# Optimization experiments

Hardware: AMD Instinct MI355X
Metric: run time of the kernel (lower is better)

## Reference

```python
import jax, jax.numpy as jnp
import numpy as np

C, H, W, N = 256, 256, 256, 512
ROI_SIZE = 7


def setup_inputs() -> dict:
    key = jax.random.key(0)
    k1, k2, k3 = jax.random.split(key, 3)
    feature = jax.random.normal(k1, (C, H, W), dtype=jnp.float32)
    # rois layout: (y1, x1, y2, x2), valid boxes inside the map
    start = jax.random.uniform(k2, (N, 2), jnp.float32, 0.0, H / 2)
    size = jax.random.uniform(k3, (N, 2), jnp.float32, 8.0, H / 2)
    rois = jnp.concatenate([start, start + size], axis=-1)
    return {"feature": feature, "rois": rois}


def _bilinear(feature, x, y):
    # feature: [C, H, W]; x, y: [...] float sample coords.
    # Faithful to the torch code: corners are clamped BEFORE computing the
    # interpolation weights (y - y1, y2 - y, etc.).
    h, w = feature.shape[-2:]
    y1 = jnp.floor(y).astype(jnp.int32)
    y2 = y1 + 1
    x1 = jnp.floor(x).astype(jnp.int32)
    x2 = x1 + 1
    y1 = jnp.clip(y1, 0, h - 1)
    y2 = jnp.clip(y2, 0, h - 1)
    x1 = jnp.clip(x1, 0, w - 1)
    x2 = jnp.clip(x2, 0, w - 1)
    wy1 = y - y1  # dist to top (clamped) corner
    wy2 = y2 - y
    wx1 = x - x1
    wx2 = x2 - x
    f11 = feature[:, y1, x1]  # [C, ...]
    f12 = feature[:, y1, x2]
    f21 = feature[:, y2, x1]
    f22 = feature[:, y2, x2]
    p = f11 * wx2 + f12 * wx1
    q = f21 * wx2 + f22 * wx1
    return p * wy2 + q * wy1


def reference(feature, rois):
    # feature: [C, H, W]; rois: [N, 4] = (y1, x1, y2, x2)
    R = ROI_SIZE
    n_roi = rois.shape[0]
    c = feature.shape[0]
    stride_h = (rois[:, 2] - rois[:, 0]) / R  # [N]
    stride_w = (rois[:, 3] - rois[:, 1]) / R  # [N]
    bins = jnp.arange(R, dtype=feature.dtype)
    y_base = rois[:, 0, None] + stride_h[:, None] * bins  # [N, 7]
    x_base = rois[:, 1, None] + stride_w[:, None] * bins  # [N, 7]
    # two sample points per bin, at 1/3 and 2/3 of the bin stride
    ys = jnp.stack([y_base + stride_h[:, None] / 3,
                    y_base + 2 * stride_h[:, None] / 3], axis=-1)  # [N, 7, 2]
    xs = jnp.stack([x_base + stride_w[:, None] / 3,
                    x_base + 2 * stride_w[:, None] / 3], axis=-1)  # [N, 7, 2]
    # all (y_sample, x_sample) combos per (roi, bin_m, bin_n): [N, 7, 7, 2, 2]
    Y = ys[:, :, None, :, None]
    X = xs[:, None, :, None, :]
    Yb, Xb = jnp.broadcast_arrays(Y, X)
    vals = _bilinear(feature, Xb, Yb)  # [C, N, 7, 7, 2, 2]
    # Faithful to torch.max(cat(...)) on a [C, 4] tensor: a GLOBAL max over
    # both channels and the 4 sample points, broadcast back to all channels.
    pooled = vals.max(axis=(0, -2, -1))  # [N, 7, 7]
    return jnp.broadcast_to(pooled[:, None, :, :], (n_roi, c, R, R))
```

## Files before the change

kernel.cpp:

```cpp
#include <hip/hip_runtime.h>

#define CCH 256
#define HH  256
#define WW  256
#define HWSZ (HH * WW)
#define NROI 512
#define RBIN 7
#define NBIN (RBIN * RBIN)
#define NTASK (2 * NBIN)
#define TFEAT_BYTES ((size_t)HWSZ * CCH * 2)

typedef float vfloat4 __attribute__((ext_vector_type(4)));

__device__ __forceinline__ unsigned short f2bf_rne(float f) {
    unsigned u = __float_as_uint(f);
    u = (u + 0x7fffu + ((u >> 16) & 1u)) >> 16;
    return (unsigned short)u;
}

__global__ __launch_bounds__(256)
void transpose_chw_to_hwc_bf16(const float* __restrict__ feat,
                               unsigned short* __restrict__ tfeat)
{
    __shared__ __align__(16) float tile[64 * 64];
    const int t   = threadIdx.x;
    const int hw0 = blockIdx.x * 64;
    const int c0  = blockIdx.y * 64;

    const int cl_r = t >> 4;
    const int fc   = t & 15;

    vfloat4 v[4];
    #pragma unroll
    for (int j = 0; j < 4; ++j) {
        v[j] = __builtin_nontemporal_load(
            (const vfloat4*)(feat + (size_t)(c0 + cl_r + j * 16) * HWSZ + hw0 + 4 * fc));
    }
    #pragma unroll
    for (int j = 0; j < 4; ++j) {
        const int cl = cl_r + j * 16;
        const int p  = (4 * fc) ^ (4 * ((cl >> 2) & 7));
        *(vfloat4*)&tile[cl * 64 + p] = v[j];
    }
    __syncthreads();

    const int cl_w = (t & 15) * 4;
    const int swz  = 4 * ((t & 15) & 7);
    #pragma unroll
    for (int j = 0; j < 4; ++j) {
        const int hl = (t >> 4) + j * 16;
        const int pc = hl ^ swz;
        ushort4 w;
        w.x = f2bf_rne(tile[(cl_w + 0) * 64 + pc]);
        w.y = f2bf_rne(tile[(cl_w + 1) * 64 + pc]);
        w.z = f2bf_rne(tile[(cl_w + 2) * 64 + pc]);
        w.w = f2bf_rne(tile[(cl_w + 3) * 64 + pc]);
        *(ushort4*)(tfeat + (size_t)(hw0 + hl) * CCH + c0 + cl_w) = w;
    }
}

__global__ __launch_bounds__(1024, 8)
void roialign_fused(const unsigned short* __restrict__ tfeat,
                    const float* __restrict__ rois,
                    float* __restrict__ out)
{
    const int n    = blockIdx.x;
    const int t    = threadIdx.x;
    const int wave = t >> 6;
    const int lane = t & 63;
    const int half = lane >> 5;
    const int cOff = (lane & 31) * 8;

    __shared__ __align__(16) float tmax[NTASK * 64];
    __shared__ float pooled[NBIN];

    const float y0 = rois[n * 4 + 0];
    const float x0 = rois[n * 4 + 1];
    const float sh = (rois[n * 4 + 2] - y0) * (1.0f / (float)RBIN);
    const float sw = (rois[n * 4 + 3] - x0) * (1.0f / (float)RBIN);

    #pragma unroll 2
    for (int task = wave; task < NTASK; task += 16) {
        const int bin = task >> 1;
        const int i   = task & 1;
        const int by  = bin / RBIN;
        const int bx  = bin - by * RBIN;

        const int point = i * 2 + half;
        const int sy = point >> 1;
        const int sx = point & 1;

        const float y = y0 + sh * (float)by +
                        ((sy == 0) ? (sh * (1.0f / 3.0f)) : (sh * (2.0f / 3.0f)));
        const float x = x0 + sw * (float)bx +
                        ((sx == 0) ? (sw * (1.0f / 3.0f)) : (sw * (2.0f / 3.0f)));

        int iy1 = (int)floorf(y);
        int iy2 = iy1 + 1;
        int ix1 = (int)floorf(x);
        int ix2 = ix1 + 1;
        iy1 = min(max(iy1, 0), HH - 1);
        iy2 = min(max(iy2, 0), HH - 1);
        ix1 = min(max(ix1, 0), WW - 1);
        ix2 = min(max(ix2, 0), WW - 1);

        const float wy1 = y - (float)iy1;
        const float wy2 = (float)iy2 - y;
        const float wx1 = x - (float)ix1;
        const float wx2 = (float)ix2 - x;

        const uint4 A = *(const uint4*)(tfeat + (size_t)(iy1 * WW + ix1) * CCH + cOff);
        const uint4 B = *(const uint4*)(tfeat + (size_t)(iy1 * WW + ix2) * CCH + cOff);
        const uint4 C = *(const uint4*)(tfeat + (size_t)(iy2 * WW + ix1) * CCH + cOff);
        const uint4 D = *(const uint4*)(tfeat + (size_t)(iy2 * WW + ix2) * CCH + cOff);
        const unsigned* ap = (const unsigned*)&A;
        const unsigned* bp = (const unsigned*)&B;
        const unsigned* cp = (const unsigned*)&C;
        const unsigned* dp = (const unsigned*)&D;

        float m = -INFINITY;
        #pragma unroll
        for (int k = 0; k < 4; ++k) {
            const unsigned ua = ap[k], ub = bp[k], uc = cp[k], ud = dp[k];
            {
                const float f11 = __uint_as_float(ua << 16);
                const float f12 = __uint_as_float(ub << 16);
                const float f21 = __uint_as_float(uc << 16);
                const float f22 = __uint_as_float(ud << 16);
                const float p = f11 * wx2 + f12 * wx1;
                const float q = f21 * wx2 + f22 * wx1;
                m = fmaxf(m, p * wy2 + q * wy1);
            }
            {
                const float f11 = __uint_as_float(ua & 0xffff0000u);
                const float f12 = __uint_as_float(ub & 0xffff0000u);
                const float f21 = __uint_as_float(uc & 0xffff0000u);
                const float f22 = __uint_as_float(ud & 0xffff0000u);
                const float p = f11 * wx2 + f12 * wx1;
                const float q = f21 * wx2 + f22 * wx1;
                m = fmaxf(m, p * wy2 + q * wy1);
            }
        }

        tmax[task * 64 + lane] = m;
    }
    __syncthreads();

    if (t < NBIN * 16) {
        const int b = t >> 4;
        const int j = t & 15;
        const float* src = &tmax[b * 128 + j * 8];
        const vfloat4 a = *(const vfloat4*)(src);
        const vfloat4 c = *(const vfloat4*)(src + 4);
        float m = fmaxf(fmaxf(fmaxf(a.x, a.y), fmaxf(a.z, a.w)),
                        fmaxf(fmaxf(c.x, c.y), fmaxf(c.z, c.w)));
        #pragma unroll
        for (int off = 8; off > 0; off >>= 1)
            m = fmaxf(m, __shfl_xor(m, off, 16));
        if (j == 0) pooled[b] = m;
    }
    __syncthreads();

    float* o = out + (size_t)n * (CCH * NBIN);
    #pragma unroll
    for (int k = 0; k < 4; ++k) {
        const int idx4 = t + k * 1024;
        if (idx4 < (CCH * NBIN) / 4) {
            int r = (idx4 * 4) % NBIN;
            vfloat4 v;
            v.x = pooled[r]; r = (r == NBIN - 1) ? 0 : r + 1;
            v.y = pooled[r]; r = (r == NBIN - 1) ? 0 : r + 1;
            v.z = pooled[r]; r = (r == NBIN - 1) ? 0 : r + 1;
            v.w = pooled[r];
            __builtin_nontemporal_store(v, (vfloat4*)o + idx4);
        }
    }
}

__global__ __launch_bounds__(256)
void roialign_direct_kernel(const float* __restrict__ feat,
                            const float* __restrict__ rois,
                            float* __restrict__ out)
{
    const int n = blockIdx.x;
    const int t = threadIdx.x;
    __shared__ float ptmax[196];
    __shared__ float pooled[NBIN];

    const float y0  = rois[n * 4 + 0];
    const float x0  = rois[n * 4 + 1];
    const float sh  = (rois[n * 4 + 2] - y0) / (float)RBIN;
    const float sw  = (rois[n * 4 + 3] - x0) / (float)RBIN;

    const bool active = (t < 196);
    int off11 = 0, off12 = 0, off21 = 0, off22 = 0;
    float wx1 = 0.f, wx2 = 0.f, wy1 = 0.f, wy2 = 0.f;
    if (active) {
        const int py = t / 14, px = t % 14;
        const int by = py >> 1, sy = py & 1;
        const int bx = px >> 1, sx = px & 1;
        const float y = y0 + sh * (float)by + ((sy == 0) ? (sh / 3.0f) : (2.0f * sh / 3.0f));
        const float x = x0 + sw * (float)bx + ((sx == 0) ? (sw / 3.0f) : (2.0f * sw / 3.0f));
        int iy1 = (int)floorf(y), iy2 = iy1 + 1;
        int ix1 = (int)floorf(x), ix2 = ix1 + 1;
        iy1 = min(max(iy1, 0), HH - 1); iy2 = min(max(iy2, 0), HH - 1);
        ix1 = min(max(ix1, 0), WW - 1); ix2 = min(max(ix2, 0), WW - 1);
        wy1 = y - (float)iy1; wy2 = (float)iy2 - y;
        wx1 = x - (float)ix1; wx2 = (float)ix2 - x;
        off11 = iy1 * WW + ix1; off12 = iy1 * WW + ix2;
        off21 = iy2 * WW + ix1; off22 = iy2 * WW + ix2;
    }
    if (active) {
        float m = -INFINITY;
        const float* f = feat;
        #pragma unroll 4
        for (int c = 0; c < CCH; ++c) {
            const float p = f[off11] * wx2 + f[off12] * wx1;
            const float q = f[off21] * wx2 + f[off22] * wx1;
            m = fmaxf(m, p * wy2 + q * wy1);
            f += HWSZ;
        }
        ptmax[t] = m;
    }
    __syncthreads();
    if (t < NBIN) {
        const int by = t / RBIN, bx = t % RBIN;
        const int p00 = (2 * by) * 14 + 2 * bx;
        pooled[t] = fmaxf(fmaxf(ptmax[p00], ptmax[p00 + 1]),
                          fmaxf(ptmax[p00 + 14], ptmax[p00 + 15]));
    }
    __syncthreads();
    float* o = out + (size_t)n * (CCH * NBIN);
    for (int idx = t; idx < CCH * NBIN; idx += 256)
        o[idx] = pooled[idx % NBIN];
}

extern "C" void kernel_launch(void* const* d_in, const int* in_sizes, int n_in,
                              void* d_out, int out_size, void* d_ws, size_t ws_size,
                              hipStream_t stream)
{
    const float* feat = (const float*)d_in[0];
    const float* rois = (const float*)d_in[1];
    float* out = (float*)d_out;

    if (ws_size < TFEAT_BYTES) {
        roialign_direct_kernel<<<NROI, 256, 0, stream>>>(feat, rois, out);
        return;
    }

    unsigned short* tfeat = (unsigned short*)d_ws;

    dim3 tgrid(HWSZ / 64, CCH / 64);
    transpose_chw_to_hwc_bf16<<<tgrid, 256, 0, stream>>>(feat, tfeat);

    roialign_fused<<<NROI, 1024, 0, stream>>>(tfeat, rois, out);
}
```

Measured before the change: 131.3 us.

## Fuse transpose and ROI pooling into one cooperative kernel with grid sync

Replaces the two-kernel sequence (CHW-to-HWC bf16 transpose, then ROI pooling) with a single cooperative launch. Each of the 512 blocks transposes 8 tiles, the grid synchronises, and then the same block pools its ROI. This removes the second kernel launch and the gap between kernels, but it runs the transpose with only 512 blocks of 1024 threads and one tile per iteration, so memory-level parallelism may drop. The old two-kernel path stays as a fallback if the cooperative launch fails.

Result: slower. 212.4 us (+61.7%).

```diff
diff --git a/kernel.cpp b/kernel.cpp
--- a/kernel.cpp
+++ b/kernel.cpp
@@ -1,4 +1,7 @@
 #include <hip/hip_runtime.h>
+#include <hip/hip_cooperative_groups.h>
+
+namespace cg = cooperative_groups;
 
 #define CCH 256
 #define HH  256
@@ -16,6 +19,163 @@
     unsigned u = __float_as_uint(f);
     u = (u + 0x7fffu + ((u >> 16) & 1u)) >> 16;
     return (unsigned short)u;
+}
+
+__global__ __launch_bounds__(1024, 8)
+void roialign_onekernel(const float* __restrict__ feat,
+                        const float* __restrict__ rois,
+                        float* __restrict__ out,
+                        unsigned short* __restrict__ tfeat)
+{
+    cg::grid_group grid = cg::this_grid();
+
+    __shared__ __align__(16) float smem[NTASK * 64];
+    __shared__ float pooled[NBIN];
+
+    const int t   = threadIdx.x;
+    const int bid = blockIdx.x;
+
+    const int n = bid;
+    const float y0 = rois[n * 4 + 0];
+    const float x0 = rois[n * 4 + 1];
+    const float sh = (rois[n * 4 + 2] - y0) * (1.0f / (float)RBIN);
+    const float sw = (rois[n * 4 + 3] - x0) * (1.0f / (float)RBIN);
+
+    {
+        const int cl  = t >> 4;
+        const int fc  = t & 15;
+        const int p   = (4 * fc) ^ (4 * ((cl >> 2) & 7));
+        const int hl  = t >> 4;
+        const int fc4 = t & 15;
+        const int cl_w = fc4 * 4;
+        const int pc   = hl ^ (4 * (fc4 & 7));
+
+        #pragma unroll 1
+        for (int it = 0; it < 8; ++it) {
+            const int tile = bid + it * NROI;
+            const int hw0  = (tile & 1023) * 64;
+            const int c0   = (tile >> 10) * 64;
+
+            const vfloat4 v = __builtin_nontemporal_load(
+                (const vfloat4*)(feat + (size_t)(c0 + cl) * HWSZ + hw0 + 4 * fc));
+            if (it) __syncthreads();
+            *(vfloat4*)&smem[cl * 64 + p] = v;
+            __syncthreads();
+
+            ushort4 w;
+            w.x = f2bf_rne(smem[(cl_w + 0) * 64 + pc]);
+            w.y = f2bf_rne(smem[(cl_w + 1) * 64 + pc]);
+            w.z = f2bf_rne(smem[(cl_w + 2) * 64 + pc]);
+            w.w = f2bf_rne(smem[(cl_w + 3) * 64 + pc]);
+            *(ushort4*)(tfeat + (size_t)(hw0 + hl) * CCH + c0 + cl_w) = w;
+        }
+    }
+
+    grid.sync();
+
+    {
+        const int wave = t >> 6;
+        const int lane = t & 63;
+        const int half = lane >> 5;
+        const int cOff = (lane & 31) * 8;
+
+        #pragma unroll 2
+        for (int task = wave; task < NTASK; task += 16) {
+            const int bin = task >> 1;
+            const int i   = task & 1;
+            const int by  = bin / RBIN;
+            const int bx  = bin - by * RBIN;
+
+            const int point = i * 2 + half;
+            const int sy = point >> 1;
+            const int sx = point & 1;
+
+            const float y = y0 + sh * (float)by +
+                            ((sy == 0) ? (sh * (1.0f / 3.0f)) : (sh * (2.0f / 3.0f)));
+            const float x = x0 + sw * (float)bx +
+                            ((sx == 0) ? (sw * (1.0f / 3.0f)) : (sw * (2.0f / 3.0f)));
+
+            int iy1 = (int)floorf(y);
+            int iy2 = iy1 + 1;
+            int ix1 = (int)floorf(x);
+            int ix2 = ix1 + 1;
+            iy1 = min(max(iy1, 0), HH - 1);
+            iy2 = min(max(iy2, 0), HH - 1);
+            ix1 = min(max(ix1, 0), WW - 1);
+            ix2 = min(max(ix2, 0), WW - 1);
+
+            const float wy1 = y - (float)iy1;
+            const float wy2 = (float)iy2 - y;
+            const float wx1 = x - (float)ix1;
+            const float wx2 = (float)ix2 - x;
+
+            const uint4 A = *(const uint4*)(tfeat + (size_t)(iy1 * WW + ix1) * CCH + cOff);
+            const uint4 B = *(const uint4*)(tfeat + (size_t)(iy1 * WW + ix2) * CCH + cOff);
+            const uint4 C = *(const uint4*)(tfeat + (size_t)(iy2 * WW + ix1) * CCH + cOff);
+            const uint4 D = *(const uint4*)(tfeat + (size_t)(iy2 * WW + ix2) * CCH + cOff);
+            const unsigned* ap = (const unsigned*)&A;
+            const unsigned* bp = (const unsigned*)&B;
+            const unsigned* cp = (const unsigned*)&C;
+            const unsigned* dp = (const unsigned*)&D;
+
+            float m = -INFINITY;
+            #pragma unroll
+            for (int k = 0; k < 4; ++k) {
+                const unsigned ua = ap[k], ub = bp[k], uc = cp[k], ud = dp[k];
+                {
+                    const float f11 = __uint_as_float(ua << 16);
+                    const float f12 = __uint_as_float(ub << 16);
+                    const float f21 = __uint_as_float(uc << 16);
+                    const float f22 = __uint_as_float(ud << 16);
+                    const float p2 = f11 * wx2 + f12 * wx1;
+                    const float q2 = f21 * wx2 + f22 * wx1;
+                    m = fmaxf(m, p2 * wy2 + q2 * wy1);
+                }
+                {
+                    const float f11 = __uint_as_float(ua & 0xffff0000u);
+                    const float f12 = __uint_as_float(ub & 0xffff0000u);
+                    const float f21 = __uint_as_float(uc & 0xffff0000u);
+                    const float f22 = __uint_as_float(ud & 0xffff0000u);
+                    const float p2 = f11 * wx2 + f12 * wx1;
+                    const float q2 = f21 * wx2 + f22 * wx1;
+                    m = fmaxf(m, p2 * wy2 + q2 * wy1);
+                }
+            }
+
+            smem[task * 64 + lane] = m;
+        }
+        __syncthreads();
+
+        if (t < NBIN * 16) {
+            const int b = t >> 4;
+            const int j = t & 15;
+            const float* src = &smem[b * 128 + j * 8];
+            const vfloat4 a = *(const vfloat4*)(src);
+            const vfloat4 c = *(const vfloat4*)(src + 4);
+            float m = fmaxf(fmaxf(fmaxf(a.x, a.y), fmaxf(a.z, a.w)),
+                            fmaxf(fmaxf(c.x, c.y), fmaxf(c.z, c.w)));
+            #pragma unroll
+            for (int off = 8; off > 0; off >>= 1)
+                m = fmaxf(m, __shfl_xor(m, off, 16));
+            if (j == 0) pooled[b] = m;
+        }
+        __syncthreads();
+
+        float* o = out + (size_t)n * (CCH * NBIN);
+        #pragma unroll
+        for (int k = 0; k < 4; ++k) {
+            const int idx4 = t + k * 1024;
+            if (idx4 < (CCH * NBIN) / 4) {
+                int r = (idx4 * 4) % NBIN;
+                vfloat4 v;
+                v.x = pooled[r]; r = (r == NBIN - 1) ? 0 : r + 1;
+                v.y = pooled[r]; r = (r == NBIN - 1) ? 0 : r + 1;
+                v.z = pooled[r]; r = (r == NBIN - 1) ? 0 : r + 1;
+                v.w = pooled[r];
+                __builtin_nontemporal_store(v, (vfloat4*)o + idx4);
+            }
+        }
+    }
 }
 
 __global__ __launch_bounds__(256)
@@ -250,8 +410,14 @@
 
     unsigned short* tfeat = (unsigned short*)d_ws;
 
+    void* args[] = { (void*)&feat, (void*)&rois, (void*)&out, (void*)&tfeat };
+    hipError_t e = hipLaunchCooperativeKernel((void*)roialign_onekernel,
+                                              dim3(NROI), dim3(1024),
+                                              args, 0, stream);
+    if (e == hipSuccess) return;
+    (void)hipGetLastError();
+
     dim3 tgrid(HWSZ / 64, CCH / 64);
     transpose_chw_to_hwc_bf16<<<tgrid, 256, 0, stream>>>(feat, tfeat);
-
     roialign_fused<<<NROI, 1024, 0, stream>>>(tfeat, rois, out);
 }
```
